# Kernel optimization log

Hardware: AMD Instinct MI355X
Metric: run time of the kernel (lower is better)

Reference implementation:

```python
import math
import jax, jax.numpy as jnp
import numpy as np

TWO_PI = 2.0 * math.pi
BETA = 1.0
K_COUP = 1.0
A_ANC = 0.08
OMEGA_ANC = TWO_PI * 200.0
B, P, N = 64, 256, 4096


def setup_inputs() -> dict:
    key = jax.random.key(0)
    k1, k2, k3 = jax.random.split(key, 3)
    t = jax.random.uniform(k1, (1,), dtype=jnp.float32)
    phi = jax.random.uniform(k2, (B, N), dtype=jnp.float32) * TWO_PI
    xi = jax.random.uniform(k3, (P, N), dtype=jnp.float32) * TWO_PI
    return {"t": t, "phi": phi, "xi": xi}


def reference(t, phi, xi):
    # diff: (B, P, N)
    diff = phi[:, None, :] - xi[None, :, :]
    m = jnp.cos(diff).sum(-1)                      # (B, P)
    weights = jax.nn.softmax(BETA * m / N, axis=-1)  # (B, P)
    coupling = jnp.einsum('bp,bpn->bn', weights, jnp.sin(diff))  # (B, N)
    dphi = K_COUP * coupling + A_ANC * jnp.sin(OMEGA_ANC * t - phi)
    return dphi
```

## Files before the change

### kernel.cpp

```cpp
#include <hip/hip_runtime.h>
#include <hip/hip_fp16.h>
#include <math.h>
#include <stdint.h>

#define B_SZ 64
#define P_SZ 256
#define N_SZ 4096
#define NCA 32
#define A_ANC 0.08f
#define OMEGA_ANC 1256.6370614359172f
#define INV_2PI 0.15915494309189535f

typedef _Float16 half8 __attribute__((ext_vector_type(8)));
typedef _Float16 half2v __attribute__((ext_vector_type(2)));
typedef float floatx4 __attribute__((ext_vector_type(4)));

__device__ __forceinline__ float vsin_r(float r) {
#if __has_builtin(__builtin_amdgcn_sinf)
    return __builtin_amdgcn_sinf(r);
#else
    return __sinf(r * 6.283185307179586f);
#endif
}
__device__ __forceinline__ float vcos_r(float r) {
#if __has_builtin(__builtin_amdgcn_cosf)
    return __builtin_amdgcn_cosf(r);
#else
    return __cosf(r * 6.283185307179586f);
#endif
}
__device__ __forceinline__ float vfract(float r) {
#if __has_builtin(__builtin_amdgcn_fractf)
    return __builtin_amdgcn_fractf(r);
#else
    return r - floorf(r);
#endif
}
__device__ __forceinline__ uint32_t cs_pack(float x) {
    float r = x * INV_2PI;
    return __builtin_bit_cast(uint32_t,
        __builtin_amdgcn_cvt_pkrtz(vcos_r(r), vsin_r(r)));
}

__device__ __forceinline__ uint32_t permsel(uint32_t hi, uint32_t lo, uint32_t sel) {
#if __has_builtin(__builtin_amdgcn_perm)
    return __builtin_amdgcn_perm(hi, lo, sel);
#else
    unsigned long long v = ((unsigned long long)hi << 32) | lo;
    uint32_t r = 0;
#pragma unroll
    for (int i = 0; i < 4; ++i)
        r |= (uint32_t)((v >> (8 * ((sel >> (8 * i)) & 7))) & 0xff) << (8 * i);
    return r;
#endif
}

__global__ __launch_bounds__(256) void k_mpart_mfma(const float* __restrict__ phi,
                                                    const float* __restrict__ xi,
                                                    uint32_t* __restrict__ XPT,
                                                    float* __restrict__ m_part) {
    const int bt = blockIdx.x & 3;
    const int pt = blockIdx.x >> 2;
    const int w  = threadIdx.x >> 6;
    const int lane = threadIdx.x & 63;
    const int m = lane & 15;
    const int q = lane >> 4;

    const int c  = blockIdx.y * 4 + w;
    const int n0 = c * 128;
    const int b_row = bt * 16 + m;
    const int p_row = pt * 16 + m;

    floatx4 acc = {0.f, 0.f, 0.f, 0.f};
#pragma unroll
    for (int s = 0; s < 8; ++s) {
        const int nb = n0 + s * 16 + q * 4;
        float4 ph = *(const float4*)&phi[b_row * N_SZ + nb];
        float4 xv = *(const float4*)&xi[p_row * N_SZ + nb];
        uint4 ai, bi;
        ai.x = cs_pack(ph.x); ai.y = cs_pack(ph.y);
        ai.z = cs_pack(ph.z); ai.w = cs_pack(ph.w);
        bi.x = cs_pack(xv.x); bi.y = cs_pack(xv.y);
        bi.z = cs_pack(xv.z); bi.w = cs_pack(xv.w);
        if (bt == 0) {
            XPT[(nb + 0) * P_SZ + p_row] = bi.x;
            XPT[(nb + 1) * P_SZ + p_row] = bi.y;
            XPT[(nb + 2) * P_SZ + p_row] = bi.z;
            XPT[(nb + 3) * P_SZ + p_row] = bi.w;
        }
        half8 af = __builtin_bit_cast(half8, ai);
        half8 bf = __builtin_bit_cast(half8, bi);
        acc = __builtin_amdgcn_mfma_f32_16x16x32_f16(af, bf, acc, 0, 0, 0);
    }
#pragma unroll
    for (int r = 0; r < 4; ++r) {
        int b = bt * 16 + q * 4 + r;
        m_part[(c * 64 + b) * 256 + pt * 16 + m] = acc[r];
    }
}

__global__ __launch_bounds__(256) void k_weights(const float* __restrict__ m_part,
                                                 _Float16* __restrict__ Wh) {
    const int b = blockIdx.x;
    const int tid = threadIdx.x;
    const int wv = tid >> 6;
    __shared__ float sred[8];

    float acc[NCA];
#pragma unroll
    for (int c = 0; c < NCA; ++c)
        acc[c] = m_part[(c * 64 + b) * 256 + tid];
    float msum = 0.f;
#pragma unroll
    for (int c = 0; c < NCA; ++c) msum += acc[c];
    float logit = msum * (1.0f / 4096.0f);

    float v = logit;
    for (int o = 32; o > 0; o >>= 1) v = fmaxf(v, __shfl_xor(v, o));
    if ((tid & 63) == 0) sred[wv] = v;
    __syncthreads();
    float mx = fmaxf(fmaxf(sred[0], sred[1]), fmaxf(sred[2], sred[3]));
    float e = __expf(logit - mx);
    v = e;
    for (int o = 32; o > 0; o >>= 1) v += __shfl_xor(v, o);
    if ((tid & 63) == 0) sred[4 + wv] = v;
    __syncthreads();
    float s = sred[4] + sred[5] + sred[6] + sred[7];
    Wh[b * 256 + tid] = (_Float16)(e / s);
}

__global__ __launch_bounds__(256) void k_coupling_mfma(const uint32_t* __restrict__ XPT,
                                                       const _Float16* __restrict__ Wh,
                                                       const float* __restrict__ phi,
                                                       const float* __restrict__ t_ptr,
                                                       float* __restrict__ out) {
    const int mt = blockIdx.x;
    const int ctg = blockIdx.y;
    const int tid = threadIdx.x;
    const int w = tid >> 6;
    const int lane = tid & 63;
    const int cl = lane & 15;
    const int q  = lane >> 4;

    __shared__ uint32_t xs[32][260];

    const int n0 = ctg * 32;
#pragma unroll
    for (int it = 0; it < 8; ++it) {
        int i = tid + it * 256;
        int row = i >> 6, seg = i & 63;
        uint4 v = *(const uint4*)&XPT[(n0 + row) * P_SZ + seg * 4];
        *(uint4*)&xs[row][seg * 4] = v;
    }
    __syncthreads();

    const int ct  = ctg * 4 + w;
    const int col = ct * 16 + cl;
    const int n   = col >> 1;
    const int n_l = w * 8 + (cl >> 1);
    const int comp = col & 1;
    const uint32_t sel = comp ? 0x07060302u : 0x05040100u;

    const _Float16* wrow = Wh + (mt * 16 + cl) * 256;

    floatx4 acc = {0.f, 0.f, 0.f, 0.f};
#pragma unroll
    for (int s = 0; s < 8; ++s) {
        const int k0 = s * 32 + q * 8;
        half8 af = *(const half8*)&wrow[k0];
        uint4 v0 = *(const uint4*)&xs[n_l][k0];
        uint4 v1 = *(const uint4*)&xs[n_l][k0 + 4];
        uint4 bi;
        bi.x = permsel(v0.y, v0.x, sel);
        bi.y = permsel(v0.w, v0.z, sel);
        bi.z = permsel(v1.y, v1.x, sel);
        bi.w = permsel(v1.w, v1.z, sel);
        half8 bf = __builtin_bit_cast(half8, bi);
        acc = __builtin_amdgcn_mfma_f32_16x16x32_f16(af, bf, acc, 0, 0, 0);
    }

    float aS0 = __shfl_xor(acc[0], 1);
    float aS1 = __shfl_xor(acc[1], 1);
    float aS2 = __shfl_xor(acc[2], 1);
    float aS3 = __shfl_xor(acc[3], 1);
    if (!comp) {
        const float wt_r = OMEGA_ANC * t_ptr[0] * INV_2PI;
        float aC[4] = {acc[0], acc[1], acc[2], acc[3]};
        float aS[4] = {aS0, aS1, aS2, aS3};
#pragma unroll
        for (int r = 0; r < 4; ++r) {
            int b = mt * 16 + q * 4 + r;
            float ph = phi[b * N_SZ + n];
            float pr = ph * INV_2PI;
            float ss = vsin_r(pr), cc = vcos_r(pr);
            float anc = vsin_r(vfract(wt_r - pr));
            out[b * N_SZ + n] = fmaf(A_ANC, anc, ss * aC[r] - cc * aS[r]);
        }
    }
}

extern "C" void kernel_launch(void* const* d_in, const int* in_sizes, int n_in,
                              void* d_out, int out_size, void* d_ws, size_t ws_size,
                              hipStream_t stream) {
    const float* t   = (const float*)d_in[0];
    const float* phi = (const float*)d_in[1];
    const float* xi  = (const float*)d_in[2];
    float* out = (float*)d_out;

    char* w = (char*)d_ws;
    uint32_t* XPT   = (uint32_t*)w;
    float* m_part   = (float*)(w + 4u * 1024 * 1024);
    _Float16* Wh    = (_Float16*)(w + 6u * 1024 * 1024);

    k_mpart_mfma<<<dim3(64, 8), 256, 0, stream>>>(phi, xi, XPT, m_part);
    k_weights<<<64, 256, 0, stream>>>(m_part, Wh);
    k_coupling_mfma<<<dim3(4, 128), 256, 0, stream>>>(XPT, Wh, phi, t, out);
}
```

Measured before the change: 75.90 us.

## Reduce m partials with atomics and fuse softmax into coupling kernel

The first kernel now accumulates its per-chunk partial m values directly into a single B×P buffer with float atomicAdd, replacing the partial-sum array and the separate reduction pass. The softmax is moved into the coupling kernel: each block computes the fp16 weights for its 16 batch rows in shared memory. This removes one kernel launch and the m_part round trip, at the cost of a memset, atomic contention, redundant softmax work repeated across 128 column blocks, and a summation order that is no longer deterministic.

```diff
diff --git a/kernel.cpp b/kernel.cpp
--- a/kernel.cpp
+++ b/kernel.cpp
@@ -6,13 +6,11 @@
 #define B_SZ 64
 #define P_SZ 256
 #define N_SZ 4096
-#define NCA 32
 #define A_ANC 0.08f
 #define OMEGA_ANC 1256.6370614359172f
 #define INV_2PI 0.15915494309189535f
 
 typedef _Float16 half8 __attribute__((ext_vector_type(8)));
-typedef _Float16 half2v __attribute__((ext_vector_type(2)));
 typedef float floatx4 __attribute__((ext_vector_type(4)));
 
 __device__ __forceinline__ float vsin_r(float r) {
@@ -58,7 +56,7 @@
 __global__ __launch_bounds__(256) void k_mpart_mfma(const float* __restrict__ phi,
                                                     const float* __restrict__ xi,
                                                     uint32_t* __restrict__ XPT,
-                                                    float* __restrict__ m_part) {
+                                                    float* __restrict__ m_total) {
     const int bt = blockIdx.x & 3;
     const int pt = blockIdx.x >> 2;
     const int w  = threadIdx.x >> 6;
@@ -95,42 +93,12 @@
 #pragma unroll
     for (int r = 0; r < 4; ++r) {
         int b = bt * 16 + q * 4 + r;
-        m_part[(c * 64 + b) * 256 + pt * 16 + m] = acc[r];
-    }
-}
-
-__global__ __launch_bounds__(256) void k_weights(const float* __restrict__ m_part,
-                                                 _Float16* __restrict__ Wh) {
-    const int b = blockIdx.x;
-    const int tid = threadIdx.x;
-    const int wv = tid >> 6;
-    __shared__ float sred[8];
-
-    float acc[NCA];
-#pragma unroll
-    for (int c = 0; c < NCA; ++c)
-        acc[c] = m_part[(c * 64 + b) * 256 + tid];
-    float msum = 0.f;
-#pragma unroll
-    for (int c = 0; c < NCA; ++c) msum += acc[c];
-    float logit = msum * (1.0f / 4096.0f);
-
-    float v = logit;
-    for (int o = 32; o > 0; o >>= 1) v = fmaxf(v, __shfl_xor(v, o));
-    if ((tid & 63) == 0) sred[wv] = v;
-    __syncthreads();
-    float mx = fmaxf(fmaxf(sred[0], sred[1]), fmaxf(sred[2], sred[3]));
-    float e = __expf(logit - mx);
-    v = e;
-    for (int o = 32; o > 0; o >>= 1) v += __shfl_xor(v, o);
-    if ((tid & 63) == 0) sred[4 + wv] = v;
-    __syncthreads();
-    float s = sred[4] + sred[5] + sred[6] + sred[7];
-    Wh[b * 256 + tid] = (_Float16)(e / s);
+        atomicAdd(&m_total[b * 256 + pt * 16 + m], acc[r]);
+    }
 }
 
 __global__ __launch_bounds__(256) void k_coupling_mfma(const uint32_t* __restrict__ XPT,
-                                                       const _Float16* __restrict__ Wh,
+                                                       const float* __restrict__ m_total,
                                                        const float* __restrict__ phi,
                                                        const float* __restrict__ t_ptr,
                                                        float* __restrict__ out) {
@@ -143,6 +111,7 @@
     const int q  = lane >> 4;
 
     __shared__ uint32_t xs[32][260];
+    __shared__ _Float16 wh[16][264];
 
     const int n0 = ctg * 32;
 #pragma unroll
@@ -151,6 +120,27 @@
         int row = i >> 6, seg = i & 63;
         uint4 v = *(const uint4*)&XPT[(n0 + row) * P_SZ + seg * 4];
         *(uint4*)&xs[row][seg * 4] = v;
+    }
+
+#pragma unroll
+    for (int j = 0; j < 4; ++j) {
+        const int bl = w * 4 + j;
+        float4 v = *(const float4*)&m_total[(mt * 16 + bl) * 256 + lane * 4];
+        float4 l = {v.x * (1.0f / 4096.0f), v.y * (1.0f / 4096.0f),
+                    v.z * (1.0f / 4096.0f), v.w * (1.0f / 4096.0f)};
+        float mx = fmaxf(fmaxf(l.x, l.y), fmaxf(l.z, l.w));
+        for (int o = 32; o > 0; o >>= 1) mx = fmaxf(mx, __shfl_xor(mx, o));
+        float e0 = __expf(l.x - mx), e1 = __expf(l.y - mx);
+        float e2 = __expf(l.z - mx), e3 = __expf(l.w - mx);
+        float s = e0 + e1 + e2 + e3;
+        for (int o = 32; o > 0; o >>= 1) s += __shfl_xor(s, o);
+        float rs = 1.0f / s;
+        uint2 pk;
+        pk.x = __builtin_bit_cast(uint32_t,
+                 __builtin_amdgcn_cvt_pkrtz(e0 * rs, e1 * rs));
+        pk.y = __builtin_bit_cast(uint32_t,
+                 __builtin_amdgcn_cvt_pkrtz(e2 * rs, e3 * rs));
+        *(uint2*)&wh[bl][lane * 4] = pk;
     }
     __syncthreads();
 
@@ -161,13 +151,11 @@
     const int comp = col & 1;
     const uint32_t sel = comp ? 0x07060302u : 0x05040100u;
 
-    const _Float16* wrow = Wh + (mt * 16 + cl) * 256;
-
     floatx4 acc = {0.f, 0.f, 0.f, 0.f};
 #pragma unroll
     for (int s = 0; s < 8; ++s) {
         const int k0 = s * 32 + q * 8;
-        half8 af = *(const half8*)&wrow[k0];
+        half8 af = *(const half8*)&wh[cl][k0];
         uint4 v0 = *(const uint4*)&xs[n_l][k0];
         uint4 v1 = *(const uint4*)&xs[n_l][k0 + 4];
         uint4 bi;
@@ -209,10 +197,9 @@
 
     char* w = (char*)d_ws;
     uint32_t* XPT   = (uint32_t*)w;
-    float* m_part   = (float*)(w + 4u * 1024 * 1024);
-    _Float16* Wh    = (_Float16*)(w + 6u * 1024 * 1024);
-
-    k_mpart_mfma<<<dim3(64, 8), 256, 0, stream>>>(phi, xi, XPT, m_part);
-    k_weights<<<64, 256, 0, stream>>>(m_part, Wh);
-    k_coupling_mfma<<<dim3(4, 128), 256, 0, stream>>>(XPT, Wh, phi, t, out);
-}
+    float* m_total  = (float*)(w + 4u * 1024 * 1024);
+
+    hipMemsetAsync(m_total, 0, B_SZ * P_SZ * sizeof(float), stream);
+    k_mpart_mfma<<<dim3(64, 8), 256, 0, stream>>>(phi, xi, XPT, m_total);
+    k_coupling_mfma<<<dim3(4, 128), 256, 0, stream>>>(XPT, m_total, phi, t, out);
+}
```

After: 75.68 us. No clear change (-0.3%).
